# Kernel optimization log

Hardware: AMD Instinct MI355X
Metric: run time of the kernel (lower is better)

## Reference

```python
import jax, jax.numpy as jnp
import numpy as np

N_NODES = 50000
N_EDGES = 800000
IN_DIM = 256
HID = 128


def setup_inputs() -> dict:
    key = jax.random.key(0)
    ks = jax.random.split(key, 8)
    x = jax.random.normal(ks[0], (N_NODES, IN_DIM), dtype=jnp.float32)
    edge_index = jax.random.randint(ks[1], (2, N_EDGES), 0, N_NODES, dtype=jnp.int32)
    edge_weight = jax.random.uniform(ks[2], (N_EDGES,), dtype=jnp.float32)
    # xavier_normal with gain=1.414 as in torch init
    g = 1.414
    W1 = jax.random.normal(ks[3], (HID, IN_DIM), dtype=jnp.float32) * (g * np.sqrt(2.0 / (HID + IN_DIM)))
    W2 = jax.random.normal(ks[4], (HID, HID), dtype=jnp.float32) * (g * np.sqrt(2.0 / (HID + HID)))
    b1 = jnp.zeros((HID,), dtype=jnp.float32)
    b2 = jnp.zeros((HID,), dtype=jnp.float32)
    a1 = jnp.full((1,), 0.25, dtype=jnp.float32)  # nn.PReLU() default init
    a2 = jnp.full((1,), 0.25, dtype=jnp.float32)
    return {"x": x, "edge_index": edge_index, "edge_weight": edge_weight,
            "W1": W1, "b1": b1, "a1": a1, "W2": W2, "b2": b2, "a2": a2}


def _gcn_layer(z, W, b, a, src, dst, w):
    # linear (no bias): [N, out]
    fts = z @ W.T
    # spmm: out[dst] += w * fts[src]
    msg = fts[src] * w[:, None]                      # [E, out]
    out = jax.ops.segment_sum(msg, dst, num_segments=N_NODES) + b
    # PReLU (single shared parameter)
    return jnp.where(out >= 0, out, a * out)


def reference(x, edge_index, edge_weight, W1, b1, a1, W2, b2, a2):
    src, dst = edge_index[0], edge_index[1]
    z = _gcn_layer(x, W1, b1, a1, src, dst, edge_weight)
    z = _gcn_layer(z, W2, b2, a2, src, dst, edge_weight)
    return z
```

## Files before the change

### kernel.cpp

```cpp
#include <hip/hip_runtime.h>

#define HID 128
#define BSH 6
#define BSZ 64
#define NBMAX 1024

typedef unsigned int uint;
typedef unsigned short ushort;
typedef __attribute__((ext_vector_type(8))) short short8;
typedef __attribute__((ext_vector_type(4))) float f32x4;

__device__ __forceinline__ uint pack_bf16x2(float a, float b) {
    uint ua = __float_as_uint(a);
    ua += 0x7fffu + ((ua >> 16) & 1u);
    uint ub = __float_as_uint(b);
    ub += 0x7fffu + ((ub >> 16) & 1u);
    return (ua >> 16) | (ub & 0xffff0000u);
}

__device__ __forceinline__ ushort bf16_of(float x) {
    uint u = __float_as_uint(x);
    u += 0x7fffu + ((u >> 16) & 1u);
    return (ushort)(u >> 16);
}

union FragAB { uint4 u; short8 s; };

__global__ __launch_bounds__(256) void w_to_frags_both(
    const float* __restrict__ W1, const float* __restrict__ W2,
    ushort* __restrict__ Wb1, ushort* __restrict__ Wb2, int* __restrict__ ghist) {
    int blk = blockIdx.x;
    if (blk == 24) {
        ((int4*)ghist)[threadIdx.x] = make_int4(0, 0, 0, 0);
        return;
    }
    const float* W = (blk < 16) ? W1 : W2;
    ushort* Wb = (blk < 16) ? Wb1 : Wb2;
    int K = (blk < 16) ? 256 : 128;
    int t = ((blk < 16) ? blk : blk - 16) * 256 + threadIdx.x;
    int lane = t & 63, f = t >> 6;
    int s = f >> 3, c = f & 7;
    int m = c * 16 + (lane & 15);
    int k0 = s * 32 + (lane >> 4) * 8;
    const float* wr = W + (size_t)m * K + k0;
    float4 a = *(const float4*)wr;
    float4 b = *(const float4*)(wr + 4);
    uint4 o = make_uint4(pack_bf16x2(a.x, a.y), pack_bf16x2(a.z, a.w),
                         pack_bf16x2(b.x, b.y), pack_bf16x2(b.z, b.w));
    *(uint4*)(Wb + (size_t)t * 8) = o;
}

template <int K, bool ABF16>
__device__ __forceinline__ FragAB load_afrag(const void* __restrict__ Xv, int row,
                                             int k0, bool ok) {
    FragAB af;
    if (ABF16) {
        af.u = ok ? *(const uint4*)((const ushort*)Xv + (size_t)row * K + k0)
                  : make_uint4(0, 0, 0, 0);
    } else {
        float4 va = make_float4(0.f, 0.f, 0.f, 0.f), vb = va;
        if (ok) {
            const float* xr = (const float*)Xv + (size_t)row * K + k0;
            va = *(const float4*)xr;
            vb = *(const float4*)(xr + 4);
        }
        af.u = make_uint4(pack_bf16x2(va.x, va.y), pack_bf16x2(va.z, va.w),
                          pack_bf16x2(vb.x, vb.y), pack_bf16x2(vb.z, vb.w));
    }
    return af;
}

template <int K, bool ABF16>
__global__ __launch_bounds__(256) void gemm_mfma(
    const void* __restrict__ Xv, const ushort* __restrict__ Wb,
    ushort* __restrict__ out, int N) {
    const int lane = threadIdx.x & 63;
    const int wid  = threadIdx.x >> 6;
    const int n0   = blockIdx.x * 128 + wid * 32;
    const int r0 = n0 + (lane & 15);
    const int r1 = r0 + 16;
    const bool ok0 = r0 < N, ok1 = r1 < N;
    const int kgrp = (lane >> 4) * 8;

    f32x4 acc0[8], acc1[8];
#pragma unroll
    for (int c = 0; c < 8; ++c) {
        acc0[c] = (f32x4){0.f, 0.f, 0.f, 0.f};
        acc1[c] = (f32x4){0.f, 0.f, 0.f, 0.f};
    }

#pragma unroll
    for (int s = 0; s < K / 32; ++s) {
        const int k0 = s * 32 + kgrp;
        FragAB a0 = load_afrag<K, ABF16>(Xv, r0, k0, ok0);
        FragAB a1 = load_afrag<K, ABF16>(Xv, r1, k0, ok1);
#pragma unroll
        for (int c = 0; c < 8; ++c) {
            FragAB bfr;
            bfr.u = *(const uint4*)(Wb + (size_t)((s * 8 + c) * 64 + lane) * 8);
            acc0[c] = __builtin_amdgcn_mfma_f32_16x16x32_bf16(a0.s, bfr.s, acc0[c], 0, 0, 0);
            acc1[c] = __builtin_amdgcn_mfma_f32_16x16x32_bf16(a1.s, bfr.s, acc1[c], 0, 0, 0);
        }
    }
    const int col = lane & 15;
    const int rb0 = n0 + (lane >> 4) * 4;
#pragma unroll
    for (int c = 0; c < 8; ++c) {
#pragma unroll
        for (int r = 0; r < 4; ++r) {
            int na = rb0 + r;
            if (na < N) out[(size_t)na * HID + c * 16 + col] = bf16_of(acc0[c][r]);
            int nb = na + 16;
            if (nb < N) out[(size_t)nb * HID + c * 16 + col] = bf16_of(acc1[c][r]);
        }
    }
}

__global__ __launch_bounds__(256) void bucket_hist(const int* __restrict__ dst,
                                                   int* __restrict__ ghist, int E, int NB) {
    __shared__ int h[NBMAX];
    for (int i = threadIdx.x; i < NB; i += 256) h[i] = 0;
    __syncthreads();
    int stride = gridDim.x * 256;
    for (int e = blockIdx.x * 256 + threadIdx.x; e < E; e += stride)
        atomicAdd(&h[dst[e] >> BSH], 1);
    __syncthreads();
    for (int i = threadIdx.x; i < NB; i += 256) {
        int c = h[i];
        if (c) atomicAdd(&ghist[i], c);
    }
}

__global__ __launch_bounds__(NBMAX) void bucket_scan(const int* __restrict__ ghist,
                                                     int* __restrict__ gbase,
                                                     int* __restrict__ gcur, int NB, int E) {
    __shared__ int l[NBMAX];
    int t = threadIdx.x;
    int v = (t < NB) ? ghist[t] : 0;
    l[t] = v;
    __syncthreads();
    int x = v;
    for (int o = 1; o < NBMAX; o <<= 1) {
        int y = (t >= o) ? l[t - o] : 0;
        __syncthreads();
        x += y;
        l[t] = x;
        __syncthreads();
    }
    if (t < NB) { gbase[t] = x - v; gcur[t] = x - v; }
    if (t == 0) gbase[NB] = E;
}

__global__ __launch_bounds__(256) void bucket_stage(
    const int* __restrict__ src, const int* __restrict__ dst,
    const float* __restrict__ w, int* __restrict__ gcur,
    int2* __restrict__ staged, int E, int NB) {
    __shared__ int lh[NBMAX], lb[NBMAX];
    for (int i = threadIdx.x; i < NB; i += 256) lh[i] = 0;
    __syncthreads();
    int chunk = (E + gridDim.x - 1) / gridDim.x;
    int c0 = blockIdx.x * chunk;
    int c1 = min(c0 + chunk, E);
    for (int e = c0 + threadIdx.x; e < c1; e += 256)
        atomicAdd(&lh[dst[e] >> BSH], 1);
    __syncthreads();
    for (int i = threadIdx.x; i < NB; i += 256) {
        int c = lh[i];
        lb[i] = c ? atomicAdd(&gcur[i], c) : 0;
        lh[i] = 0;
    }
    __syncthreads();
    for (int e = c0 + threadIdx.x; e < c1; e += 256) {
        int d = dst[e];
        int b = d >> BSH;
        int slot = lb[b] + atomicAdd(&lh[b], 1);
        staged[slot] = make_int2(src[e] | ((d & (BSZ - 1)) << 16), __float_as_int(w[e]));
    }
}

__global__ __launch_bounds__(256) void node_sort(
    const int* __restrict__ gbase, const int2* __restrict__ staged,
    int2* __restrict__ csr, int* __restrict__ off, int N) {
    __shared__ int hist[BSZ];
    __shared__ int cur[BSZ];
    const int b = blockIdx.x;
    const int s0 = gbase[b], s1 = gbase[b + 1];
    const int t = threadIdx.x;
    if (t < BSZ) hist[t] = 0;
    __syncthreads();
    for (int e = s0 + t; e < s1; e += 256)
        atomicAdd(&hist[(staged[e].x >> 16) & (BSZ - 1)], 1);
    __syncthreads();
    if (t < BSZ) {
        int x = hist[t];
        int incl = x;
#pragma unroll
        for (int o = 1; o < BSZ; o <<= 1) {
            int y = __shfl_up(incl, o, BSZ);
            if (t >= o) incl += y;
        }
        int excl = incl - x;
        cur[t] = excl;
        int n = (b << BSH) + t;
        if (n <= N) off[n] = s0 + excl;
    }
    __syncthreads();
    for (int e = s0 + t; e < s1; e += 256) {
        int2 m = staged[e];
        int d = (m.x >> 16) & (BSZ - 1);
        int p = atomicAdd(&cur[d], 1);
        csr[s0 + p] = m;
    }
}

template <bool OUTBF16>
__global__ __launch_bounds__(256) void csr_gather_bf16(
    const int* __restrict__ off, const int2* __restrict__ edges,
    const ushort* __restrict__ fts, void* __restrict__ outv,
    const float* __restrict__ bias, const float* __restrict__ alpha, int N) {
    int d = blockIdx.x * 4 + (threadIdx.x >> 6);
    if (d >= N) return;
    const int lane = threadIdx.x & 63;
    const int g = lane >> 4;
    const int sub = lane & 15;
    int p = off[d];
    const int end = off[d + 1];
    float acc[8];
#pragma unroll
    for (int j = 0; j < 8; ++j) acc[j] = 0.f;

#define LOBITS(u_) __uint_as_float((u_) << 16)
#define HIBITS(u_) __uint_as_float((u_) & 0xffff0000u)
#define ACC8(R_, W_)                                              \
    do {                                                          \
        acc[0] += (W_) * LOBITS((R_).x); acc[1] += (W_) * HIBITS((R_).x); \
        acc[2] += (W_) * LOBITS((R_).y); acc[3] += (W_) * HIBITS((R_).y); \
        acc[4] += (W_) * LOBITS((R_).z); acc[5] += (W_) * HIBITS((R_).z); \
        acc[6] += (W_) * LOBITS((R_).w); acc[7] += (W_) * HIBITS((R_).w); \
    } while (0)

    for (; p + 8 <= end; p += 8) {
        int2 ma = edges[p + g];
        int2 mb = edges[p + 4 + g];
        uint4 ra = *(const uint4*)(fts + (size_t)(ma.x & 0xffff) * HID + sub * 8);
        uint4 rb = *(const uint4*)(fts + (size_t)(mb.x & 0xffff) * HID + sub * 8);
        float wa = __int_as_float(ma.y), wb = __int_as_float(mb.y);
        ACC8(ra, wa);
        ACC8(rb, wb);
    }
    for (; p < end; p += 4) {
        int i = p + g;
        int2 m = edges[(i < end) ? i : (end - 1)];
        float wt = (i < end) ? __int_as_float(m.y) : 0.f;
        uint4 r = *(const uint4*)(fts + (size_t)(m.x & 0xffff) * HID + sub * 8);
        ACC8(r, wt);
    }
#undef ACC8
#undef LOBITS
#undef HIBITS

#pragma unroll
    for (int j = 0; j < 8; ++j) {
        acc[j] += __shfl_xor(acc[j], 16);
        acc[j] += __shfl_xor(acc[j], 32);
    }

    const float a = alpha[0];
#pragma unroll
    for (int j = 0; j < 8; ++j) {
        float v = acc[j] + bias[sub * 8 + j];
        acc[j] = v >= 0.f ? v : a * v;
    }
    if (g == 0) {
        if (OUTBF16) {
            uint4 o = make_uint4(pack_bf16x2(acc[0], acc[1]), pack_bf16x2(acc[2], acc[3]),
                                 pack_bf16x2(acc[4], acc[5]), pack_bf16x2(acc[6], acc[7]));
            *(uint4*)((ushort*)outv + (size_t)d * HID + sub * 8) = o;
        } else {
            float* op = (float*)outv + (size_t)d * HID + sub * 8;
            *(float4*)op = make_float4(acc[0], acc[1], acc[2], acc[3]);
            *(float4*)(op + 4) = make_float4(acc[4], acc[5], acc[6], acc[7]);
        }
    }
}

extern "C" void kernel_launch(void* const* d_in, const int* in_sizes, int n_in,
                              void* d_out, int out_size, void* d_ws, size_t ws_size,
                              hipStream_t stream) {
    const float* x  = (const float*)d_in[0];
    const int*   ei = (const int*)d_in[1];
    const float* ew = (const float*)d_in[2];
    const float* W1 = (const float*)d_in[3];
    const float* b1 = (const float*)d_in[4];
    const float* a1 = (const float*)d_in[5];
    const float* W2 = (const float*)d_in[6];
    const float* b2 = (const float*)d_in[7];
    const float* a2 = (const float*)d_in[8];
    float* out = (float*)d_out;

    int N = in_sizes[0] / 256;
    int E = in_sizes[2];
    const int* src = ei;
    const int* dst = ei + E;
    int NB = (N + BSZ - 1) >> BSH;

    ushort* fts    = (ushort*)d_ws;
    ushort* agg    = fts + (size_t)N * HID;
    int2*   staged = (int2*)(agg + (size_t)N * HID);
    int2*   csr    = staged + E;
    ushort* Wb1    = (ushort*)(csr + E);
    ushort* Wb2    = Wb1 + 128 * 256;
    int*    ghist  = (int*)(Wb2 + 128 * 128);
    int*    gbase  = ghist + NBMAX;
    int*    gcur   = gbase + NBMAX + 1;
    int*    off    = gcur + NBMAX;

    w_to_frags_both<<<25, 256, 0, stream>>>(W1, W2, Wb1, Wb2, ghist);

    bucket_hist<<<256, 256, 0, stream>>>(dst, ghist, E, NB);
    bucket_scan<<<1, NBMAX, 0, stream>>>(ghist, gbase, gcur, NB, E);
    bucket_stage<<<128, 256, 0, stream>>>(src, dst, ew, gcur, staged, E, NB);
    node_sort<<<NB, 256, 0, stream>>>(gbase, staged, csr, off, N);

    int gblk = (N + 127) / 128;
    int ggrid = (N + 3) / 4;

    gemm_mfma<256, false><<<gblk, 256, 0, stream>>>(x, Wb1, fts, N);
    csr_gather_bf16<true><<<ggrid, 256, 0, stream>>>(off, csr, fts, agg, b1, a1, N);

    gemm_mfma<128, true><<<gblk, 256, 0, stream>>>(agg, Wb2, fts, N);
    csr_gather_bf16<false><<<ggrid, 256, 0, stream>>>(off, csr, fts, out, b2, a2, N);
}
```

Before: 153.0 us.

## Fuse histogram into weight-pack kernel with per-block partials; unroll gather by 16

New measurement: 154.0 us. Within noise of the previous version (+0.7%).

```diff
diff --git a/kernel.cpp b/kernel.cpp
--- a/kernel.cpp
+++ b/kernel.cpp
@@ -1,37 +1,44 @@
 #include <hip/hip_runtime.h>
+#include <hip/hip_bf16.h>
 
 #define HID 128
 #define BSH 6
 #define BSZ 64
 #define NBMAX 1024
+#define HB 64
 
 typedef unsigned int uint;
 typedef unsigned short ushort;
 typedef __attribute__((ext_vector_type(8))) short short8;
 typedef __attribute__((ext_vector_type(4))) float f32x4;
 
+__device__ __forceinline__ ushort bf16_of(float x) {
+    return __bfloat16_as_ushort(__float2bfloat16(x));
+}
+
 __device__ __forceinline__ uint pack_bf16x2(float a, float b) {
-    uint ua = __float_as_uint(a);
-    ua += 0x7fffu + ((ua >> 16) & 1u);
-    uint ub = __float_as_uint(b);
-    ub += 0x7fffu + ((ub >> 16) & 1u);
-    return (ua >> 16) | (ub & 0xffff0000u);
-}
-
-__device__ __forceinline__ ushort bf16_of(float x) {
-    uint u = __float_as_uint(x);
-    u += 0x7fffu + ((u >> 16) & 1u);
-    return (ushort)(u >> 16);
+    return (uint)bf16_of(a) | ((uint)bf16_of(b) << 16);
 }
 
 union FragAB { uint4 u; short8 s; };
 
-__global__ __launch_bounds__(256) void w_to_frags_both(
+__global__ __launch_bounds__(256) void pack_hist(
     const float* __restrict__ W1, const float* __restrict__ W2,
-    ushort* __restrict__ Wb1, ushort* __restrict__ Wb2, int* __restrict__ ghist) {
+    ushort* __restrict__ Wb1, ushort* __restrict__ Wb2,
+    const int* __restrict__ dst, int* __restrict__ hpart, int E, int NB) {
     int blk = blockIdx.x;
-    if (blk == 24) {
-        ((int4*)ghist)[threadIdx.x] = make_int4(0, 0, 0, 0);
+    if (blk >= 24) {
+        __shared__ int h[NBMAX];
+        int hb = blk - 24;
+        for (int i = threadIdx.x; i < NB; i += 256) h[i] = 0;
+        __syncthreads();
+        int chunk = (E + HB - 1) / HB;
+        int c0 = hb * chunk;
+        int c1 = min(c0 + chunk, E);
+        for (int e = c0 + threadIdx.x; e < c1; e += 256)
+            atomicAdd(&h[dst[e] >> BSH], 1);
+        __syncthreads();
+        for (int i = threadIdx.x; i < NB; i += 256) hpart[hb * NBMAX + i] = h[i];
         return;
     }
     const float* W = (blk < 16) ? W1 : W2;
@@ -116,27 +123,14 @@
     }
 }
 
-__global__ __launch_bounds__(256) void bucket_hist(const int* __restrict__ dst,
-                                                   int* __restrict__ ghist, int E, int NB) {
-    __shared__ int h[NBMAX];
-    for (int i = threadIdx.x; i < NB; i += 256) h[i] = 0;
-    __syncthreads();
-    int stride = gridDim.x * 256;
-    for (int e = blockIdx.x * 256 + threadIdx.x; e < E; e += stride)
-        atomicAdd(&h[dst[e] >> BSH], 1);
-    __syncthreads();
-    for (int i = threadIdx.x; i < NB; i += 256) {
-        int c = h[i];
-        if (c) atomicAdd(&ghist[i], c);
-    }
-}
-
-__global__ __launch_bounds__(NBMAX) void bucket_scan(const int* __restrict__ ghist,
+__global__ __launch_bounds__(NBMAX) void bucket_scan(const int* __restrict__ hpart,
                                                      int* __restrict__ gbase,
                                                      int* __restrict__ gcur, int NB, int E) {
     __shared__ int l[NBMAX];
     int t = threadIdx.x;
-    int v = (t < NB) ? ghist[t] : 0;
+    int v = 0;
+    if (t < NB)
+        for (int b = 0; b < HB; ++b) v += hpart[b * NBMAX + t];
     l[t] = v;
     __syncthreads();
     int x = v;
@@ -231,6 +225,7 @@
 
 #define LOBITS(u_) __uint_as_float((u_) << 16)
 #define HIBITS(u_) __uint_as_float((u_) & 0xffff0000u)
+#define ROWOF(M_) (*(const uint4*)(fts + (size_t)((M_).x & 0xffff) * HID + sub * 8))
 #define ACC8(R_, W_)                                              \
     do {                                                          \
         acc[0] += (W_) * LOBITS((R_).x); acc[1] += (W_) * HIBITS((R_).x); \
@@ -239,11 +234,18 @@
         acc[6] += (W_) * LOBITS((R_).w); acc[7] += (W_) * HIBITS((R_).w); \
     } while (0)
 
+    for (; p + 16 <= end; p += 16) {
+        int2 m0 = edges[p + g], m1 = edges[p + 4 + g];
+        int2 m2 = edges[p + 8 + g], m3 = edges[p + 12 + g];
+        uint4 r0 = ROWOF(m0), r1 = ROWOF(m1), r2 = ROWOF(m2), r3 = ROWOF(m3);
+        float w0 = __int_as_float(m0.y), w1 = __int_as_float(m1.y);
+        float w2 = __int_as_float(m2.y), w3 = __int_as_float(m3.y);
+        ACC8(r0, w0); ACC8(r1, w1); ACC8(r2, w2); ACC8(r3, w3);
+    }
     for (; p + 8 <= end; p += 8) {
         int2 ma = edges[p + g];
         int2 mb = edges[p + 4 + g];
-        uint4 ra = *(const uint4*)(fts + (size_t)(ma.x & 0xffff) * HID + sub * 8);
-        uint4 rb = *(const uint4*)(fts + (size_t)(mb.x & 0xffff) * HID + sub * 8);
+        uint4 ra = ROWOF(ma), rb = ROWOF(mb);
         float wa = __int_as_float(ma.y), wb = __int_as_float(mb.y);
         ACC8(ra, wa);
         ACC8(rb, wb);
@@ -252,10 +254,11 @@
         int i = p + g;
         int2 m = edges[(i < end) ? i : (end - 1)];
         float wt = (i < end) ? __int_as_float(m.y) : 0.f;
-        uint4 r = *(const uint4*)(fts + (size_t)(m.x & 0xffff) * HID + sub * 8);
+        uint4 r = ROWOF(m);
         ACC8(r, wt);
     }
 #undef ACC8
+#undef ROWOF
 #undef LOBITS
 #undef HIBITS
 
@@ -310,15 +313,14 @@
     int2*   csr    = staged + E;
     ushort* Wb1    = (ushort*)(csr + E);
     ushort* Wb2    = Wb1 + 128 * 256;
-    int*    ghist  = (int*)(Wb2 + 128 * 128);
-    int*    gbase  = ghist + NBMAX;
+    int*    hpart  = (int*)(Wb2 + 128 * 128);
+    int*    gbase  = hpart + HB * NBMAX;
     int*    gcur   = gbase + NBMAX + 1;
     int*    off    = gcur + NBMAX;
 
-    w_to_frags_both<<<25, 256, 0, stream>>>(W1, W2, Wb1, Wb2, ghist);
-
-    bucket_hist<<<256, 256, 0, stream>>>(dst, ghist, E, NB);
-    bucket_scan<<<1, NBMAX, 0, stream>>>(ghist, gbase, gcur, NB, E);
+    pack_hist<<<24 + HB, 256, 0, stream>>>(W1, W2, Wb1, Wb2, dst, hpart, E, NB);
+
+    bucket_scan<<<1, NBMAX, 0, stream>>>(hpart, gbase, gcur, NB, E);
     bucket_stage<<<128, 256, 0, stream>>>(src, dst, ew, gcur, staged, E, NB);
     node_sort<<<NB, 256, 0, stream>>>(gbase, staged, csr, off, N);
 
```
